# Performance work log

Measured on AMD Instinct MI355X. Metric: run time of the kernel, lower is better.

## Reference

```python
import jax, jax.numpy as jnp
import numpy as np

DIM = 768
HEADS = 12
B, N = 1, 4096


def setup_inputs() -> dict:
    key = jax.random.key(0)
    k1, k2, k3 = jax.random.split(key, 3)
    x = jax.random.normal(k1, (B, N, DIM), dtype=jnp.float32)
    W_qkv = jax.random.normal(k2, (DIM, 3 * DIM), dtype=jnp.float32) * (DIM ** -0.5)
    W_out = jax.random.normal(k3, (DIM, DIM), dtype=jnp.float32) * (DIM ** -0.5)
    b_out = jnp.zeros((DIM,), dtype=jnp.float32)
    return {"x": x, "W_qkv": W_qkv, "W_out": W_out, "b_out": b_out}


def reference(x, W_qkv, W_out, b_out):
    b, n, dim = x.shape
    h = HEADS
    d = dim // h
    qkv = x @ W_qkv  # [b, n, 3*dim]
    q, k, v = jnp.split(qkv, 3, axis=-1)
    # 'b n (h d) -> b h n d'
    def to_heads(a):
        return a.reshape(b, n, h, d).transpose(0, 2, 1, 3)
    q, k, v = to_heads(q), to_heads(k), to_heads(v)
    # NOTE: original module computes self.scale but never applies it -> unscaled dots
    dots = jnp.einsum('bhid,bhjd->bhij', q, k)
    attn = jax.nn.softmax(dots, axis=-1)
    out = jnp.einsum('bhij,bhjd->bhid', attn, v)
    out = out.transpose(0, 2, 1, 3).reshape(b, n, dim)  # 'b h n d -> b n (h d)'
    return out @ W_out + b_out
```

## Files before the change

### kernel.cpp

```cpp
#include <hip/hip_runtime.h>

typedef unsigned short ushort_t;
typedef unsigned int uint_t;
typedef __bf16 bf16x8 __attribute__((ext_vector_type(8)));
typedef __bf16 bf16x4 __attribute__((ext_vector_type(4)));
typedef float f32x4 __attribute__((ext_vector_type(4)));
typedef ushort_t u16x4 __attribute__((ext_vector_type(4)));

#define NSEQ 4096
#define DIMM 768
#define NQKV 2304
#define HEADS 12
#define LOG2E 1.4426950408889634f

#if __has_builtin(__builtin_amdgcn_exp2f)
#define EXP2(x) __builtin_amdgcn_exp2f(x)
#else
#define EXP2(x) exp2f(x)
#endif


__device__ __forceinline__ ushort_t f2bf(float f) {
    uint_t u = __float_as_uint(f);
    u = u + 0x7fffu + ((u >> 16) & 1u);
    return (ushort_t)(u >> 16);
}
__device__ __forceinline__ f32x4 zero4() {
    f32x4 v = {0.f, 0.f, 0.f, 0.f};
    return v;
}

__device__ __forceinline__ void pack_w_tile(const float* __restrict__ src,
                                            ushort_t* __restrict__ dst,
                                            int K, int N, int bk, int bn, int t,
                                            ushort_t* Ls) {
    const int tr = t >> 4, tc = t & 15;
#pragma unroll
    for (int i = 0; i < 4; ++i) {
        int r = tr + 16 * i;
        float4 v = *(const float4*)(&src[(size_t)(bk + r) * N + bn + tc * 4]);
        const float* vv = (const float*)&v;
#pragma unroll
        for (int j = 0; j < 4; ++j) Ls[(tc * 4 + j) * 72 + r] = f2bf(vv[j]);
    }
    __syncthreads();
    const int KB = K >> 3;
    const int n = t >> 2;
    const int ks = t & 3;
    const int gn = bn + n;
    size_t base = ((size_t)(gn >> 4) * KB + ((bk + ks * 16) >> 3)) * 128 + (gn & 15) * 8;
    *(uint4*)(&dst[base])       = *(const uint4*)(&Ls[n * 72 + ks * 16]);
    *(uint4*)(&dst[base + 128]) = *(const uint4*)(&Ls[n * 72 + ks * 16 + 8]);
}

#define CVT_BLOCKS   3072
#define PW1_BLOCKS   (12 * 36)
#define PW2_BLOCKS   (12 * 12)

__global__ __launch_bounds__(256) void prep_kernel(
    const float* __restrict__ X, const float* __restrict__ Wqkv, const float* __restrict__ Wout,
    ushort_t* __restrict__ Ap, ushort_t* __restrict__ Wqp, ushort_t* __restrict__ Wop)
{
    __shared__ ushort_t Ls[64 * 72];
    const int b = blockIdx.x;
    const int t = threadIdx.x;
    if (b < CVT_BLOCKS) {
        int i = b * 256 + t;
        int row = i / (DIMM / 4);
        int k0 = (i - row * (DIMM / 4)) * 4;
        float4 v = *(const float4*)(&X[(size_t)row * DIMM + k0]);
        u16x4 p = { f2bf(v.x), f2bf(v.y), f2bf(v.z), f2bf(v.w) };
        size_t idx = ((size_t)(row >> 4) * (DIMM / 8) + (k0 >> 3)) * 128 + (row & 15) * 8 + (k0 & 7);
        *(u16x4*)(&Ap[idx]) = p;
    } else if (b < CVT_BLOCKS + PW1_BLOCKS) {
        int j = b - CVT_BLOCKS;
        pack_w_tile(Wqkv, Wqp, DIMM, NQKV, (j % 12) * 64, (j / 12) * 64, t, Ls);
    } else {
        int j = b - CVT_BLOCKS - PW1_BLOCKS;
        pack_w_tile(Wout, Wop, DIMM, DIMM, (j % 12) * 64, (j / 12) * 64, t, Ls);
    }
}

#define QKV_LOAD(af, bfv, kt) do {                                                            \
    _Pragma("unroll")                                                                         \
    for (int mi = 0; mi < 4; ++mi)                                                            \
        af[mi] = *(const bf16x8*)(&Ap[((size_t)(amb + mi) * KB + (kt) * 4 + g) * 128 + m16 * 8]); \
    _Pragma("unroll")                                                                         \
    for (int nj = 0; nj < 4; ++nj)                                                            \
        bfv[nj] = *(const bf16x8*)(&Bp[((size_t)(bnb + nj) * KB + (kt) * 4 + g) * 128 + m16 * 8]); \
} while (0)

__global__ __launch_bounds__(256) void qkv_gemm_kernel(
    const ushort_t* __restrict__ Ap, const ushort_t* __restrict__ Bp,
    ushort_t* __restrict__ Qp, ushort_t* __restrict__ Kp, ushort_t* __restrict__ Vp)
{
    const int t = threadIdx.x;
    const int lane = t & 63;
    const int w = t >> 6;
    const int m16 = lane & 15;
    const int g = lane >> 4;
    const int wrow = (w >> 1) * 64;
    const int wcol = (w & 1) * 64;
    const int bm = blockIdx.y * 128;
    const int bn = blockIdx.x * 128;
    const int amb = (bm + wrow) >> 4;
    const int bnb = (bn + wcol) >> 4;
    const int KB = DIMM / 8;
    const int which = bn / DIMM;

    f32x4 acc[4][4];
#pragma unroll
    for (int i = 0; i < 4; ++i)
#pragma unroll
        for (int j = 0; j < 4; ++j) acc[i][j] = zero4();

    bf16x8 af0[4], bf0[4], af1[4], bf1[4];
    QKV_LOAD(af0, bf0, 0);

    if (which < 2) {
        for (int kt = 0; kt < 24; kt += 2) {
            QKV_LOAD(af1, bf1, kt + 1);
#pragma unroll
            for (int mi = 0; mi < 4; ++mi)
#pragma unroll
                for (int nj = 0; nj < 4; ++nj)
                    acc[mi][nj] = __builtin_amdgcn_mfma_f32_16x16x32_bf16(bf0[nj], af0[mi], acc[mi][nj], 0, 0, 0);
            if (kt + 2 < 24) QKV_LOAD(af0, bf0, kt + 2);
#pragma unroll
            for (int mi = 0; mi < 4; ++mi)
#pragma unroll
                for (int nj = 0; nj < 4; ++nj)
                    acc[mi][nj] = __builtin_amdgcn_mfma_f32_16x16x32_bf16(bf1[nj], af1[mi], acc[mi][nj], 0, 0, 0);
        }
        ushort_t* dst = (which == 0) ? Qp : Kp;
        const float scale = (which == 0) ? LOG2E : 1.0f;
        const int cb = bn - which * DIMM + wcol;
        const int h = cb >> 6;
        const int ghi = g >> 1, glo = g & 1;
#pragma unroll
        for (int mi = 0; mi < 4; ++mi) {
            int sblk = amb + mi;
#pragma unroll
            for (int nj = 0; nj < 4; ++nj) {
                size_t idx = (((size_t)h * 256 + sblk) * 8 + nj * 2 + ghi) * 128 + m16 * 8 + glo * 4;
                u16x4 pk = { f2bf(acc[mi][nj][0] * scale), f2bf(acc[mi][nj][1] * scale),
                             f2bf(acc[mi][nj][2] * scale), f2bf(acc[mi][nj][3] * scale) };
                *(u16x4*)(&dst[idx]) = pk;
            }
        }
    } else {
        for (int kt = 0; kt < 24; kt += 2) {
            QKV_LOAD(af1, bf1, kt + 1);
#pragma unroll
            for (int mi = 0; mi < 4; ++mi)
#pragma unroll
                for (int nj = 0; nj < 4; ++nj)
                    acc[mi][nj] = __builtin_amdgcn_mfma_f32_16x16x32_bf16(af0[mi], bf0[nj], acc[mi][nj], 0, 0, 0);
            if (kt + 2 < 24) QKV_LOAD(af0, bf0, kt + 2);
#pragma unroll
            for (int mi = 0; mi < 4; ++mi)
#pragma unroll
                for (int nj = 0; nj < 4; ++nj)
                    acc[mi][nj] = __builtin_amdgcn_mfma_f32_16x16x32_bf16(af1[mi], bf1[nj], acc[mi][nj], 0, 0, 0);
        }
        const int cb = bn - 2 * DIMM + wcol;
        const int h = cb >> 6;
        const int ghi = g >> 1, glo = g & 1;
        const int kb8 = (bm + wrow) >> 3;
#pragma unroll
        for (int mi = 0; mi < 4; ++mi) {
#pragma unroll
            for (int nj = 0; nj < 4; ++nj) {
                size_t idx = (((size_t)h * 512 + kb8 + mi * 2 + ghi) * 4 + nj) * 128 + m16 * 8 + glo * 4;
                u16x4 pk = { f2bf(acc[mi][nj][0]), f2bf(acc[mi][nj][1]),
                             f2bf(acc[mi][nj][2]), f2bf(acc[mi][nj][3]) };
                *(u16x4*)(&Vp[idx]) = pk;
            }
        }
    }
}

#define ATTN_LOADK(dst, ptr) do {                          \
    dst[0][0] = *(const bf16x8*)(ptr);                     \
    dst[0][1] = *(const bf16x8*)((ptr) + 512);             \
    dst[1][0] = *(const bf16x8*)((ptr) + 1024);            \
    dst[1][1] = *(const bf16x8*)((ptr) + 1536);            \
} while (0)

#define ATTN_LOADV(dst, ptr) do {                          \
    dst[0] = *(const bf16x8*)(ptr);                        \
    dst[1] = *(const bf16x8*)((ptr) + 128);                \
    dst[2] = *(const bf16x8*)((ptr) + 256);                \
    dst[3] = *(const bf16x8*)((ptr) + 384);                \
} while (0)

__global__ __launch_bounds__(128, 3) void attn_kernel(
    const ushort_t* __restrict__ Qp, const ushort_t* __restrict__ Kp,
    const ushort_t* __restrict__ Vp, float* __restrict__ Opart, float* __restrict__ Lpart,
    int niter)
{
    __shared__ ushort_t Ps[2][64 * 40];
    const int t = threadIdx.x;
    const int lane = t & 63;
    const int w = t >> 6;
    const int m16 = lane & 15;
    const int g = lane >> 4;
    const int h = blockIdx.y;
    const int half = blockIdx.z;
    const int qb = blockIdx.x * 128 + w * 64;
    const int qblk0 = qb >> 4;
    const int kblk0 = half * niter * 4;
    const int vblk0 = half * niter * 8;

    bf16x8 qf[4][2];
#pragma unroll
    for (int mi = 0; mi < 4; ++mi)
#pragma unroll
        for (int kd = 0; kd < 2; ++kd)
            qf[mi][kd] = *(const bf16x8*)(&Qp[(((size_t)h * 256 + qblk0 + mi) * 8 + kd * 4 + g) * 128 + m16 * 8]);

    const ushort_t* kp = Kp + ((size_t)h * 256 + kblk0) * 1024 + g * 128 + m16 * 8;
    const ushort_t* vp = Vp + ((size_t)h * 512 + vblk0) * 512 + g * 512 + m16 * 8;

    f32x4 oacc[4][4];
#pragma unroll
    for (int mi = 0; mi < 4; ++mi)
#pragma unroll
        for (int dj = 0; dj < 4; ++dj) oacc[mi][dj] = zero4();
    f32x4 lacc[4] = {zero4(), zero4(), zero4(), zero4()};

    const int nsteps = niter * 2;
    for (int s = 0; s < nsteps; ++s) {
        bf16x8 kf[2][2], vf[4];
        ATTN_LOADK(kf, kp); kp += 2048;
        ATTN_LOADV(vf, vp); vp += 2048;
        asm volatile("" ::: "memory");
#pragma unroll
        for (int mi = 0; mi < 4; ++mi) {
#pragma unroll
            for (int nj = 0; nj < 2; ++nj) {
                f32x4 st = zero4();
                st = __builtin_amdgcn_mfma_f32_16x16x32_bf16(kf[nj][0], qf[mi][0], st, 0, 0, 0);
                st = __builtin_amdgcn_mfma_f32_16x16x32_bf16(kf[nj][1], qf[mi][1], st, 0, 0, 0);
                f32x4 p;
#pragma unroll
                for (int r = 0; r < 4; ++r) p[r] = EXP2(st[r]);
                lacc[mi] += p;
                bf16x4 pk = { (__bf16)p[0], (__bf16)p[1], (__bf16)p[2], (__bf16)p[3] };
                *(bf16x4*)(&Ps[w][(mi * 16 + m16) * 40 + nj * 16 + g * 4]) = pk;
            }
            bf16x8 pf = *(const bf16x8*)(&Ps[w][(mi * 16 + m16) * 40 + g * 8]);
#pragma unroll
            for (int dj = 0; dj < 4; ++dj)
                oacc[mi][dj] = __builtin_amdgcn_mfma_f32_16x16x32_bf16(pf, vf[dj], oacc[mi][dj], 0, 0, 0);
        }
    }

    float* Oph = Opart + (size_t)half * NSEQ * DIMM;
    float* Lph = Lpart + (size_t)half * HEADS * NSEQ + (size_t)h * NSEQ;
#pragma unroll
    for (int mi = 0; mi < 4; ++mi) {
        float l = (lacc[mi][0] + lacc[mi][1]) + (lacc[mi][2] + lacc[mi][3]);
        l += __shfl_xor(l, 16);
        l += __shfl_xor(l, 32);
        if (g == 0) Lph[qb + mi * 16 + m16] = l;
    }
#pragma unroll
    for (int mi = 0; mi < 4; ++mi) {
#pragma unroll
        for (int r = 0; r < 4; ++r) {
            int row = qb + mi * 16 + g * 4 + r;
#pragma unroll
            for (int dj = 0; dj < 4; ++dj)
                Oph[(size_t)row * DIMM + h * 64 + dj * 16 + m16] = oacc[mi][dj][r];
        }
    }
}

__global__ __launch_bounds__(256) void merge_kernel(
    const float* __restrict__ Opart, const float* __restrict__ Lpart,
    ushort_t* __restrict__ Xap, int nsplit)
{
    int i = blockIdx.x * 256 + threadIdx.x;
    int row = i / (DIMM / 4);
    int col0 = (i - row * (DIMM / 4)) * 4;
    int h = col0 >> 6;
    float l = 0.f;
    f32x4 o = zero4();
    for (int s = 0; s < nsplit; ++s) {
        l += Lpart[(size_t)s * HEADS * NSEQ + (size_t)h * NSEQ + row];
        f32x4 ov = *(const f32x4*)(&Opart[(size_t)s * NSEQ * DIMM + (size_t)row * DIMM + col0]);
        o += ov;
    }
    float inv = 1.0f / l;
    u16x4 p = { f2bf(o[0] * inv), f2bf(o[1] * inv), f2bf(o[2] * inv), f2bf(o[3] * inv) };
    size_t idx = ((size_t)(row >> 4) * (DIMM / 8) + (col0 >> 3)) * 128 + (row & 15) * 8 + (col0 & 7);
    *(u16x4*)(&Xap[idx]) = p;
}

__global__ __launch_bounds__(64, 4) void out_gemm_kernel(
    const ushort_t* __restrict__ Ap, const ushort_t* __restrict__ Bp,
    const float* __restrict__ bias, float* __restrict__ out)
{
    const int lane = threadIdx.x & 63;
    const int m16 = lane & 15;
    const int g = lane >> 4;
    const int bm = blockIdx.y * 32;
    const int bn = blockIdx.x * 64;
    const int amb = bm >> 4;
    const int bnb = bn >> 4;
    const int KB = DIMM / 8;

    f32x4 acc[2][4];
#pragma unroll
    for (int i = 0; i < 2; ++i)
#pragma unroll
        for (int j = 0; j < 4; ++j) acc[i][j] = zero4();

#pragma unroll 2
    for (int kt = 0; kt < 24; ++kt) {
        bf16x8 af[2], bfv[4];
#pragma unroll
        for (int mi = 0; mi < 2; ++mi)
            af[mi] = *(const bf16x8*)(&Ap[((size_t)(amb + mi) * KB + kt * 4 + g) * 128 + m16 * 8]);
#pragma unroll
        for (int nj = 0; nj < 4; ++nj)
            bfv[nj] = *(const bf16x8*)(&Bp[((size_t)(bnb + nj) * KB + kt * 4 + g) * 128 + m16 * 8]);
#pragma unroll
        for (int mi = 0; mi < 2; ++mi)
#pragma unroll
            for (int nj = 0; nj < 4; ++nj)
                acc[mi][nj] = __builtin_amdgcn_mfma_f32_16x16x32_bf16(af[mi], bfv[nj], acc[mi][nj], 0, 0, 0);
    }
#pragma unroll
    for (int mi = 0; mi < 2; ++mi) {
#pragma unroll
        for (int nj = 0; nj < 4; ++nj) {
            int col = bn + nj * 16 + m16;
            float bv = bias[col];
#pragma unroll
            for (int r = 0; r < 4; ++r) {
                int row = bm + mi * 16 + g * 4 + r;
                out[(size_t)row * DIMM + col] = acc[mi][nj][r] + bv;
            }
        }
    }
}

extern "C" void kernel_launch(void* const* d_in, const int* in_sizes, int n_in,
                              void* d_out, int out_size, void* d_ws, size_t ws_size,
                              hipStream_t stream) {
    (void)in_sizes; (void)n_in; (void)out_size;
    const float* X    = (const float*)d_in[0];
    const float* Wqkv = (const float*)d_in[1];
    const float* Wout = (const float*)d_in[2];
    const float* bout = (const float*)d_in[3];
    float* out = (float*)d_out;

    const size_t TSZ = (size_t)NSEQ * DIMM;
    const size_t fixed = TSZ * 2 * 5 + (size_t)NQKV * DIMM * 2 + (size_t)DIMM * DIMM * 2;
    const size_t per_split = TSZ * 4 + (size_t)HEADS * NSEQ * 4;
    const int nsplit = (ws_size >= fixed + 4 * per_split) ? 4 : 2;

    unsigned char* p = (unsigned char*)d_ws;
    ushort_t* Ap  = (ushort_t*)p; p += TSZ * 2;
    ushort_t* Wqp = (ushort_t*)p; p += (size_t)NQKV * DIMM * 2;
    ushort_t* Wop = (ushort_t*)p; p += (size_t)DIMM * DIMM * 2;
    ushort_t* Qp  = (ushort_t*)p; p += TSZ * 2;
    ushort_t* Kp  = (ushort_t*)p; p += TSZ * 2;
    ushort_t* Vp  = (ushort_t*)p; p += TSZ * 2;
    ushort_t* Xap = (ushort_t*)p; p += TSZ * 2;
    float* Opart  = (float*)p;    p += (size_t)nsplit * TSZ * 4;
    float* Lpart  = (float*)p;

    const int niter = (NSEQ / 64) / nsplit;

    prep_kernel<<<CVT_BLOCKS + PW1_BLOCKS + PW2_BLOCKS, 256, 0, stream>>>(X, Wqkv, Wout, Ap, Wqp, Wop);
    qkv_gemm_kernel<<<dim3(NQKV / 128, NSEQ / 128), 256, 0, stream>>>(Ap, Wqp, Qp, Kp, Vp);
    attn_kernel<<<dim3(NSEQ / 128, HEADS, nsplit), 128, 0, stream>>>(Qp, Kp, Vp, Opart, Lpart, niter);
    merge_kernel<<<TSZ / 4 / 256, 256, 0, stream>>>(Opart, Lpart, Xap, nsplit);
    out_gemm_kernel<<<dim3(DIMM / 64, NSEQ / 32), 64, 0, stream>>>(Xap, Wop, bout, out);
}
```

Measured before the change: 195.8 us.

## Double-buffer K through LDS via async global_load_lds and prefetch V registers

The attention inner loop now streams K tiles into a per-wave double-buffered LDS staging area with global_load_lds and prefetches the next V fragments into alternating register sets, using explicit vmcnt waits to overlap loads with MFMA work. The step is split into half-steps with s_setprio raised around MFMA groups, and the row-sum accumulator becomes a scalar. The aim is to hide global memory latency in the attention loop, at the cost of extra LDS and registers that may reduce occupancy. The final loop iteration issues a prefetch past the end of the range, which could read out of bounds.

New measurement: 271.4 us. +38.6%, slower.

```diff
diff --git a/kernel.cpp b/kernel.cpp
--- a/kernel.cpp
+++ b/kernel.cpp
@@ -28,6 +28,12 @@
 __device__ __forceinline__ f32x4 zero4() {
     f32x4 v = {0.f, 0.f, 0.f, 0.f};
     return v;
+}
+
+__device__ __forceinline__ void gload_lds16(const ushort_t* g, ushort_t* l) {
+    __builtin_amdgcn_global_load_lds(
+        (const __attribute__((address_space(1))) void*)g,
+        (__attribute__((address_space(3))) void*)l, 16, 0, 0);
 }
 
 __device__ __forceinline__ void pack_w_tile(const float* __restrict__ src,
@@ -180,18 +186,63 @@
     }
 }
 
-#define ATTN_LOADK(dst, ptr) do {                          \
-    dst[0][0] = *(const bf16x8*)(ptr);                     \
-    dst[0][1] = *(const bf16x8*)((ptr) + 512);             \
-    dst[1][0] = *(const bf16x8*)((ptr) + 1024);            \
-    dst[1][1] = *(const bf16x8*)((ptr) + 1536);            \
+#define ATTN_PREFETCH(VF, KBUF) do {                                         \
+    _Pragma("unroll")                                                        \
+    for (int dj = 0; dj < 4; ++dj)                                           \
+        VF[dj] = *(const bf16x8*)(vp + dj * 128);                            \
+    vp += 2048;                                                              \
+    _Pragma("unroll")                                                        \
+    for (int j = 0; j < 4; ++j)                                              \
+        gload_lds16(ksrc + j * 512, &Kst[w][KBUF][j * 512]);                 \
+    ksrc += 2048;                                                            \
 } while (0)
 
-#define ATTN_LOADV(dst, ptr) do {                          \
-    dst[0] = *(const bf16x8*)(ptr);                        \
-    dst[1] = *(const bf16x8*)((ptr) + 128);                \
-    dst[2] = *(const bf16x8*)((ptr) + 256);                \
-    dst[3] = *(const bf16x8*)((ptr) + 384);                \
+#define ATTN_STEP(KBUF, VF) do {                                                              \
+    const ushort_t* kb_ = &Kst[w][KBUF][lane * 8];                                            \
+    bf16x8 kf_[2][2];                                                                         \
+    kf_[0][0] = *(const bf16x8*)(kb_);                                                        \
+    kf_[0][1] = *(const bf16x8*)(kb_ + 512);                                                  \
+    kf_[1][0] = *(const bf16x8*)(kb_ + 1024);                                                 \
+    kf_[1][1] = *(const bf16x8*)(kb_ + 1536);                                                 \
+    _Pragma("unroll")                                                                         \
+    for (int hp = 0; hp < 2; ++hp) {                                                          \
+        f32x4 st_[2][2];                                                                      \
+        __builtin_amdgcn_s_setprio(1);                                                        \
+        _Pragma("unroll")                                                                     \
+        for (int i = 0; i < 2; ++i) {                                                         \
+            _Pragma("unroll")                                                                 \
+            for (int nj = 0; nj < 2; ++nj) {                                                  \
+                f32x4 x = zero4();                                                            \
+                x = __builtin_amdgcn_mfma_f32_16x16x32_bf16(kf_[nj][0], qf[hp * 2 + i][0], x, 0, 0, 0); \
+                x = __builtin_amdgcn_mfma_f32_16x16x32_bf16(kf_[nj][1], qf[hp * 2 + i][1], x, 0, 0, 0); \
+                st_[i][nj] = x;                                                               \
+            }                                                                                 \
+        }                                                                                     \
+        __builtin_amdgcn_s_setprio(0);                                                        \
+        _Pragma("unroll")                                                                     \
+        for (int i = 0; i < 2; ++i) {                                                         \
+            _Pragma("unroll")                                                                 \
+            for (int nj = 0; nj < 2; ++nj) {                                                  \
+                f32x4 p_;                                                                     \
+                _Pragma("unroll")                                                             \
+                for (int r = 0; r < 4; ++r) p_[r] = EXP2(st_[i][nj][r]);                      \
+                lacc[hp * 2 + i] += (p_[0] + p_[1]) + (p_[2] + p_[3]);                        \
+                bf16x4 pk_ = { (__bf16)p_[0], (__bf16)p_[1], (__bf16)p_[2], (__bf16)p_[3] };  \
+                *(bf16x4*)(&Ps[w][((hp * 2 + i) * 16 + m16) * 40 + nj * 16 + g * 4]) = pk_;   \
+            }                                                                                 \
+        }                                                                                     \
+        bf16x8 pf_[2];                                                                        \
+        _Pragma("unroll")                                                                     \
+        for (int i = 0; i < 2; ++i)                                                           \
+            pf_[i] = *(const bf16x8*)(&Ps[w][((hp * 2 + i) * 16 + m16) * 40 + g * 8]);        \
+        __builtin_amdgcn_s_setprio(1);                                                        \
+        _Pragma("unroll")                                                                     \
+        for (int i = 0; i < 2; ++i)                                                           \
+            _Pragma("unroll")                                                                 \
+            for (int dj = 0; dj < 4; ++dj)                                                    \
+                oacc[hp * 2 + i][dj] = __builtin_amdgcn_mfma_f32_16x16x32_bf16(pf_[i], VF[dj], oacc[hp * 2 + i][dj], 0, 0, 0); \
+        __builtin_amdgcn_s_setprio(0);                                                        \
+    }                                                                                         \
 } while (0)
 
 __global__ __launch_bounds__(128, 3) void attn_kernel(
@@ -199,6 +250,7 @@
     const ushort_t* __restrict__ Vp, float* __restrict__ Opart, float* __restrict__ Lpart,
     int niter)
 {
+    __shared__ ushort_t Kst[2][2][2048];
     __shared__ ushort_t Ps[2][64 * 40];
     const int t = threadIdx.x;
     const int lane = t & 63;
@@ -219,7 +271,7 @@
         for (int kd = 0; kd < 2; ++kd)
             qf[mi][kd] = *(const bf16x8*)(&Qp[(((size_t)h * 256 + qblk0 + mi) * 8 + kd * 4 + g) * 128 + m16 * 8]);
 
-    const ushort_t* kp = Kp + ((size_t)h * 256 + kblk0) * 1024 + g * 128 + m16 * 8;
+    const ushort_t* ksrc = Kp + ((size_t)h * 256 + kblk0) * 1024 + lane * 8;
     const ushort_t* vp = Vp + ((size_t)h * 512 + vblk0) * 512 + g * 512 + m16 * 8;
 
     f32x4 oacc[4][4];
@@ -227,40 +279,27 @@
     for (int mi = 0; mi < 4; ++mi)
 #pragma unroll
         for (int dj = 0; dj < 4; ++dj) oacc[mi][dj] = zero4();
-    f32x4 lacc[4] = {zero4(), zero4(), zero4(), zero4()};
+    float lacc[4] = {0.f, 0.f, 0.f, 0.f};
 
     const int nsteps = niter * 2;
-    for (int s = 0; s < nsteps; ++s) {
-        bf16x8 kf[2][2], vf[4];
-        ATTN_LOADK(kf, kp); kp += 2048;
-        ATTN_LOADV(vf, vp); vp += 2048;
-        asm volatile("" ::: "memory");
-#pragma unroll
-        for (int mi = 0; mi < 4; ++mi) {
-#pragma unroll
-            for (int nj = 0; nj < 2; ++nj) {
-                f32x4 st = zero4();
-                st = __builtin_amdgcn_mfma_f32_16x16x32_bf16(kf[nj][0], qf[mi][0], st, 0, 0, 0);
-                st = __builtin_amdgcn_mfma_f32_16x16x32_bf16(kf[nj][1], qf[mi][1], st, 0, 0, 0);
-                f32x4 p;
-#pragma unroll
-                for (int r = 0; r < 4; ++r) p[r] = EXP2(st[r]);
-                lacc[mi] += p;
-                bf16x4 pk = { (__bf16)p[0], (__bf16)p[1], (__bf16)p[2], (__bf16)p[3] };
-                *(bf16x4*)(&Ps[w][(mi * 16 + m16) * 40 + nj * 16 + g * 4]) = pk;
-            }
-            bf16x8 pf = *(const bf16x8*)(&Ps[w][(mi * 16 + m16) * 40 + g * 8]);
-#pragma unroll
-            for (int dj = 0; dj < 4; ++dj)
-                oacc[mi][dj] = __builtin_amdgcn_mfma_f32_16x16x32_bf16(pf, vf[dj], oacc[mi][dj], 0, 0, 0);
-        }
-    }
+    bf16x8 vA[4], vB[4];
+    ATTN_PREFETCH(vA, 0);
+
+    for (int s = 0; s < nsteps; s += 2) {
+        ATTN_PREFETCH(vB, 1);
+        asm volatile("s_waitcnt vmcnt(8)" ::: "memory");
+        ATTN_STEP(0, vA);
+        ATTN_PREFETCH(vA, 0);
+        asm volatile("s_waitcnt vmcnt(8)" ::: "memory");
+        ATTN_STEP(1, vB);
+    }
+    asm volatile("s_waitcnt vmcnt(0)" ::: "memory");
 
     float* Oph = Opart + (size_t)half * NSEQ * DIMM;
     float* Lph = Lpart + (size_t)half * HEADS * NSEQ + (size_t)h * NSEQ;
 #pragma unroll
     for (int mi = 0; mi < 4; ++mi) {
-        float l = (lacc[mi][0] + lacc[mi][1]) + (lacc[mi][2] + lacc[mi][3]);
+        float l = lacc[mi];
         l += __shfl_xor(l, 16);
         l += __shfl_xor(l, 32);
         if (g == 0) Lph[qb + mi * 16 + m16] = l;
```

## Stage QKV GEMM tiles through LDS with async global_load_lds double buffering

Applied to the files above, without the earlier changes.

The QKV projection GEMM now copies A and B tiles into double-buffered shared memory with direct global-to-LDS loads, and fragments are read from LDS. Before, each wave loaded its own fragments straight from global memory into registers. Sharing tiles across the four waves is meant to halve redundant global traffic and cut register pressure from double-buffered register fragments. In exchange it adds a block-wide barrier per k-step and 32KB of LDS per block, which may lower occupancy.

New measurement: 190.3 us. -2.8%, faster.

```diff
diff --git a/kernel.cpp b/kernel.cpp
--- a/kernel.cpp
+++ b/kernel.cpp
@@ -28,6 +28,12 @@
 __device__ __forceinline__ f32x4 zero4() {
     f32x4 v = {0.f, 0.f, 0.f, 0.f};
     return v;
+}
+
+__device__ __forceinline__ void gload_lds16(const ushort_t* g, ushort_t* l) {
+    __builtin_amdgcn_global_load_lds(
+        (const __attribute__((address_space(1))) void*)g,
+        (__attribute__((address_space(3))) void*)l, 16, 0, 0);
 }
 
 __device__ __forceinline__ void pack_w_tile(const float* __restrict__ src,
@@ -81,19 +87,27 @@
     }
 }
 
-#define QKV_LOAD(af, bfv, kt) do {                                                            \
-    _Pragma("unroll")                                                                         \
-    for (int mi = 0; mi < 4; ++mi)                                                            \
-        af[mi] = *(const bf16x8*)(&Ap[((size_t)(amb + mi) * KB + (kt) * 4 + g) * 128 + m16 * 8]); \
-    _Pragma("unroll")                                                                         \
-    for (int nj = 0; nj < 4; ++nj)                                                            \
-        bfv[nj] = *(const bf16x8*)(&Bp[((size_t)(bnb + nj) * KB + (kt) * 4 + g) * 128 + m16 * 8]); \
+#define QKV_STAGE(buf, kt) do {                                          \
+    gload_lds16(asrc0 + (kt) * 512, &As[buf][(w * 2)     * 512]);        \
+    gload_lds16(asrc1 + (kt) * 512, &As[buf][(w * 2 + 1) * 512]);        \
+    gload_lds16(bsrc0 + (kt) * 512, &Bs[buf][(w * 2)     * 512]);        \
+    gload_lds16(bsrc1 + (kt) * 512, &Bs[buf][(w * 2 + 1) * 512]);        \
 } while (0)
+
+#define QKV_FRAGS(cur) \
+    bf16x8 af[4], bfv[4];                                                \
+    _Pragma("unroll")                                                    \
+    for (int mi = 0; mi < 4; ++mi)                                       \
+        af[mi] = *(const bf16x8*)(&As[cur][aoff + mi * 512 + lfr]);      \
+    _Pragma("unroll")                                                    \
+    for (int nj = 0; nj < 4; ++nj)                                       \
+        bfv[nj] = *(const bf16x8*)(&Bs[cur][boff + nj * 512 + lfr]);
 
 __global__ __launch_bounds__(256) void qkv_gemm_kernel(
     const ushort_t* __restrict__ Ap, const ushort_t* __restrict__ Bp,
     ushort_t* __restrict__ Qp, ushort_t* __restrict__ Kp, ushort_t* __restrict__ Vp)
 {
+    __shared__ ushort_t As[2][4096], Bs[2][4096];
     const int t = threadIdx.x;
     const int lane = t & 63;
     const int w = t >> 6;
@@ -105,32 +119,39 @@
     const int bn = blockIdx.x * 128;
     const int amb = (bm + wrow) >> 4;
     const int bnb = (bn + wcol) >> 4;
+    const int bm16 = bm >> 4;
+    const int bn16 = bn >> 4;
     const int KB = DIMM / 8;
     const int which = bn / DIMM;
 
+    const ushort_t* asrc0 = Ap + ((size_t)(bm16 + w * 2)     * KB) * 128 + lane * 8;
+    const ushort_t* asrc1 = Ap + ((size_t)(bm16 + w * 2 + 1) * KB) * 128 + lane * 8;
+    const ushort_t* bsrc0 = Bp + ((size_t)(bn16 + w * 2)     * KB) * 128 + lane * 8;
+    const ushort_t* bsrc1 = Bp + ((size_t)(bn16 + w * 2 + 1) * KB) * 128 + lane * 8;
+    const int aoff = (w >> 1) * 2048;
+    const int boff = (w & 1) * 2048;
+    const int lfr = g * 128 + m16 * 8;
+
     f32x4 acc[4][4];
 #pragma unroll
     for (int i = 0; i < 4; ++i)
 #pragma unroll
         for (int j = 0; j < 4; ++j) acc[i][j] = zero4();
 
-    bf16x8 af0[4], bf0[4], af1[4], bf1[4];
-    QKV_LOAD(af0, bf0, 0);
+    QKV_STAGE(0, 0);
+    __syncthreads();
 
     if (which < 2) {
-        for (int kt = 0; kt < 24; kt += 2) {
-            QKV_LOAD(af1, bf1, kt + 1);
+        for (int kt = 0; kt < 24; ++kt) {
+            const int cur = kt & 1;
+            if (kt + 1 < 24) QKV_STAGE(cur ^ 1, kt + 1);
+            QKV_FRAGS(cur);
 #pragma unroll
             for (int mi = 0; mi < 4; ++mi)
 #pragma unroll
                 for (int nj = 0; nj < 4; ++nj)
-                    acc[mi][nj] = __builtin_amdgcn_mfma_f32_16x16x32_bf16(bf0[nj], af0[mi], acc[mi][nj], 0, 0, 0);
-            if (kt + 2 < 24) QKV_LOAD(af0, bf0, kt + 2);
-#pragma unroll
-            for (int mi = 0; mi < 4; ++mi)
-#pragma unroll
-                for (int nj = 0; nj < 4; ++nj)
-                    acc[mi][nj] = __builtin_amdgcn_mfma_f32_16x16x32_bf16(bf1[nj], af1[mi], acc[mi][nj], 0, 0, 0);
+                    acc[mi][nj] = __builtin_amdgcn_mfma_f32_16x16x32_bf16(bfv[nj], af[mi], acc[mi][nj], 0, 0, 0);
+            __syncthreads();
         }
         ushort_t* dst = (which == 0) ? Qp : Kp;
         const float scale = (which == 0) ? LOG2E : 1.0f;
@@ -149,19 +170,16 @@
             }
         }
     } else {
-        for (int kt = 0; kt < 24; kt += 2) {
-            QKV_LOAD(af1, bf1, kt + 1);
+        for (int kt = 0; kt < 24; ++kt) {
+            const int cur = kt & 1;
+            if (kt + 1 < 24) QKV_STAGE(cur ^ 1, kt + 1);
+            QKV_FRAGS(cur);
 #pragma unroll
             for (int mi = 0; mi < 4; ++mi)
 #pragma unroll
                 for (int nj = 0; nj < 4; ++nj)
-                    acc[mi][nj] = __builtin_amdgcn_mfma_f32_16x16x32_bf16(af0[mi], bf0[nj], acc[mi][nj], 0, 0, 0);
-            if (kt + 2 < 24) QKV_LOAD(af0, bf0, kt + 2);
-#pragma unroll
-            for (int mi = 0; mi < 4; ++mi)
-#pragma unroll
-                for (int nj = 0; nj < 4; ++nj)
-                    acc[mi][nj] = __builtin_amdgcn_mfma_f32_16x16x32_bf16(af1[mi], bf1[nj], acc[mi][nj], 0, 0, 0);
+                    acc[mi][nj] = __builtin_amdgcn_mfma_f32_16x16x32_bf16(af[mi], bfv[nj], acc[mi][nj], 0, 0, 0);
+            __syncthreads();
         }
         const int cb = bn - 2 * DIMM + wcol;
         const int h = cb >> 6;
```
